# Performance work log

Hardware: AMD Instinct MI355X
Metric: run time of the kernel (lower is better)

Reference implementation:

```python
import jax, jax.numpy as jnp
import numpy as np

D = 100  # embedding_dim (hard-coded in the original module)


def _prelu(x, a):
    return jnp.where(x >= 0, x, a * x)


def setup_inputs() -> dict:
    key = jax.random.key(0)
    ks = jax.random.split(key, 12)
    B, S, L, R, V = 32, 50, 20, 16, 50000
    T = L * R  # tokens per sentence = len_max_sentence * n_routes
    return {
        "stories": jax.random.randint(ks[0], (B, S, T), 0, V),
        "queries": jax.random.randint(ks[1], (B, L), 0, V),
        "emb": 0.1 * jax.random.normal(ks[2], (V, D), dtype=jnp.float32),
        "in_mult": jnp.ones((T, D), dtype=jnp.float32),
        "q_mult": jnp.ones((L, D), dtype=jnp.float32),
        "keys": 0.1 * jax.random.normal(ks[3], (R, D), dtype=jnp.float32),
        "init_state": 0.1 * jax.random.normal(ks[4], (D,), dtype=jnp.float32),
        "U": 0.1 * jax.random.normal(ks[5], (R * D, D), dtype=jnp.float32),
        "Vw": 0.1 * jax.random.normal(ks[6], (R * D, R * D), dtype=jnp.float32),
        "Ww": 0.1 * jax.random.normal(ks[7], (R * D, R * D), dtype=jnp.float32),
        "Hw": 0.1 * jax.random.normal(ks[8], (D, D), dtype=jnp.float32),
        "Rw": 0.1 * jax.random.normal(ks[9], (V, D), dtype=jnp.float32),
        "alpha_in": jnp.ones((1,), dtype=jnp.float32),  # PReLU(init=1)
        "alpha_q": jnp.ones((1,), dtype=jnp.float32),
    }


def reference(stories, queries, emb, in_mult, q_mult, keys, init_state,
              U, Vw, Ww, Hw, Rw, alpha_in, alpha_q):
    B, S, T = stories.shape
    R = keys.shape[0]
    emb0 = emb.at[0].set(0.0)  # padding_idx=0 row is zero
    # stories -> [B,S,T,D] -> route-sum -> [B,S,R,D]
    x = emb0[stories] * in_mult
    x = x.reshape(B, S, R, T // R, D).sum(axis=3)
    # V(keys.flatten()) is constant across timesteps
    v_keys = (keys.reshape(-1) @ Vw.T).reshape(R, D)
    state0 = jnp.tile(init_state[None, None, :], (B, 1, 1))  # [B,1,D]

    def step(state, sent):  # state [B,1,D], sent [B,R,D]
        gate = jax.nn.sigmoid(sent * state + sent * keys)
        u = (state.reshape(B, D) @ U.T).reshape(B, R, D)
        w = (sent.reshape(B, R * D) @ Ww.T).reshape(B, R, D)
        cand = _prelu(u + v_keys + w, alpha_in)
        # null-sentence mask: zero out positions where gate == sigmoid(0) = 0.5
        mask = jax.lax.stop_gradient(jnp.where(gate == 0.5, 0.0, 1.0))
        state = state + (cand * gate * mask).sum(axis=1, keepdims=True)
        # torch.norm over singleton dim=1 (= elementwise abs), kept faithful
        state = state / jnp.sqrt(jnp.sum(state * state, axis=1, keepdims=True))
        return state, None

    state, _ = jax.lax.scan(step, state0, jnp.swapaxes(x, 0, 1))

    q = (emb0[queries] * q_mult).sum(axis=1, keepdims=True)  # [B,1,D]
    h = _prelu(q + (state.reshape(B, D) @ Hw.T).reshape(B, 1, D), alpha_q)
    return h.reshape(B, D) @ Rw.T  # [B, vocab]
```

## Files before the change

kernel.cpp:

```cpp
#include <hip/hip_runtime.h>
#include <cstddef>
#include <cstdint>

#define B_  32
#define S_  50
#define L_  20
#define R_  16
#define D_  100
#define V_  50000
#define T_  320
#define RD_ 1600
#define BS_ 1600
#define NG_ 25
#define NP_ 16

typedef float v4f __attribute__((ext_vector_type(4)));
typedef unsigned short u16;
#define NTL(p)   __builtin_nontemporal_load((const v4f*)(p))

__device__ __forceinline__ void bsplit(float a, unsigned& h, unsigned& l) {
  const unsigned bits = __float_as_uint(a);
  const unsigned hb = bits & 0xffff0000u;
  h = hb >> 16;
  l = __float_as_uint(a - __uint_as_float(hb)) >> 16;
}

__device__ __forceinline__ void bsplit4(float4 a, uint2& h, uint2& l) {
  unsigned h0,h1,h2,h3,l0,l1,l2,l3;
  bsplit(a.x, h0, l0); bsplit(a.y, h1, l1);
  bsplit(a.z, h2, l2); bsplit(a.w, h3, l3);
  h.x = h0 | (h1 << 16); h.y = h2 | (h3 << 16);
  l.x = l0 | (l1 << 16); l.y = l2 | (l3 << 16);
}

__global__ __launch_bounds__(512) void setup_kernel(
    const int* __restrict__ stories, const float* __restrict__ emb,
    const float* __restrict__ in_mult, const float* __restrict__ U,
    const float* __restrict__ Vw, const float* __restrict__ keys,
    const float* __restrict__ init_state, const float* __restrict__ Ww,
    float* __restrict__ x,
    u16* __restrict__ wh, u16* __restrict__ wl,
    float* __restrict__ table, float* __restrict__ vk, float* __restrict__ u0)
{
  const int blk = blockIdx.x, tid = threadIdx.x;
  if (blk < 1600) {
    __shared__ int toks[T_];
    const int* st = stories + (size_t)blk * T_;
    if (tid < T_) toks[tid] = st[tid];
    __syncthreads();
    if (tid < 400) {
      const int j4 = tid * 4;
      const int r  = j4 / D_;
      const int d4 = j4 - r * D_;
      float4 acc = make_float4(0.f, 0.f, 0.f, 0.f);
      #pragma unroll
      for (int l = 0; l < 20; ++l) {
        const int t = r * 20 + l;
        const int tok = toks[t];
        if (tok != 0) {
          float4 e = *(const float4*)&emb[(size_t)tok * D_ + d4];
          float4 m = *(const float4*)&in_mult[(size_t)t * D_ + d4];
          acc.x += e.x * m.x; acc.y += e.y * m.y;
          acc.z += e.z * m.z; acc.w += e.w * m.w;
        }
      }
      float* xo = x + (size_t)blk * RD_;
      xo[(d4 + 0) * 16 + r] = acc.x;
      xo[(d4 + 1) * 16 + r] = acc.y;
      xo[(d4 + 2) * 16 + r] = acc.z;
      xo[(d4 + 3) * 16 + r] = acc.w;
    }
  } else if (blk < 2000) {
    const int qq = blk - 1600;
    const int g = qq >> 4, p = qq & 15;
    const float s0 = (p & 1) ? -1.f : 1.f;
    const float s1 = (p & 2) ? -1.f : 1.f;
    const float s2 = (p & 4) ? -1.f : 1.f;
    const float s3 = (p & 8) ? -1.f : 1.f;
    if (tid < 400) {
      const int d  = tid >> 2;
      const int r0 = (tid & 3) * 4;
      float t[4];
      #pragma unroll
      for (int ri = 0; ri < 4; ++ri) {
        const int orig = (r0 + ri) * D_ + d;
        const float* ur = &U[(size_t)orig * D_ + 4 * g];
        t[ri] = s0*ur[0] + s1*ur[1] + s2*ur[2] + s3*ur[3];
      }
      *(float4*)&table[((size_t)(g * NP_ + p)) * RD_ + tid * 4] =
          make_float4(t[0], t[1], t[2], t[3]);
    }
  } else if (blk < 2200) {
    const int wave = tid >> 6, lane = tid & 63;
    const int jp = (blk - 2000) * 8 + wave;
    const int orig = (jp & 15) * D_ + (jp >> 4);
    float acc = 0.f;
    for (int k = lane; k < RD_; k += 64)
      acc += keys[k] * Vw[(size_t)orig * RD_ + k];
    #pragma unroll
    for (int off = 32; off > 0; off >>= 1) acc += __shfl_down(acc, off);
    if (lane == 0) vk[jp] = acc;
  } else if (blk < 2400) {
    const int wave = tid >> 6, lane = tid & 63;
    const int jp = (blk - 2200) * 8 + wave;
    const int orig = (jp & 15) * D_ + (jp >> 4);
    const float* Ur = U + (size_t)orig * D_;
    float acc = Ur[lane] * init_state[lane];
    if (lane < 36) acc += Ur[64 + lane] * init_state[64 + lane];
    #pragma unroll
    for (int off = 32; off > 0; off >>= 1) acc += __shfl_down(acc, off);
    if (lane == 0) u0[jp] = acc;
  } else {
    const int g   = (blk - 2400) * 512 + tid;
    const int row = g / 200;
    const int rem = g - row * 200;
    const int d   = rem % 100;
    const int r0  = (rem / 100) * 8;
    const int orig = (row & 15) * D_ + (row >> 4);
    const float* src = Ww + (size_t)orig * RD_;
    unsigned h[8], l[8];
    #pragma unroll
    for (int i = 0; i < 8; ++i)
      bsplit(src[(r0 + i) * D_ + d], h[i], l[i]);
    uint4 hv = make_uint4(h[0]|(h[1]<<16), h[2]|(h[3]<<16),
                          h[4]|(h[5]<<16), h[6]|(h[7]<<16));
    uint4 lv = make_uint4(l[0]|(l[1]<<16), l[2]|(l[3]<<16),
                          l[4]|(l[5]<<16), l[6]|(l[7]<<16));
    *(uint4*)&wh[(size_t)row * RD_ + d * 16 + r0] = hv;
    *(uint4*)&wl[(size_t)row * RD_ + d * 16 + r0] = lv;
  }
}

typedef const __attribute__((address_space(1))) unsigned GAu;
typedef __attribute__((address_space(3))) unsigned LDSu;
#define GLL(SRC, DST) __builtin_amdgcn_global_load_lds((GAu*)(SRC), (LDSu*)(DST), 16, 0, 0)

__device__ __forceinline__ void mfma16(v4f& d, v4f a, v4f b) {
  asm("v_mfma_f32_16x16x32_bf16 %0, %1, %2, %0" : "+v"(d) : "v"(a), "v"(b));
}

__global__ __launch_bounds__(512) void gemm_mfma_kernel(
    const float* __restrict__ A,
    const u16* __restrict__ wh, const u16* __restrict__ wl,
    float* __restrict__ C)
{
  __shared__ __align__(16) char smem[2][4][8192];
  const int tid = threadIdx.x;
  const int lane = tid & 63, wid = tid >> 6;
  const int bm = blockIdx.y * 128, bn = blockIdx.x * 128;

  const int brow = wid * 16 + (lane >> 2);
  const int bkb  = (lane & 3) * 16;
  int rb = bn + brow; if (rb > 1599) rb = 1599;
  const int srcB = rb * 3200 + bkb;
  const int ldsB = wid * 1024;
  const char* gwh = (const char*)wh;
  const char* gwl = (const char*)wl;

  int arow[2], awofs[2];
  const int akseg = tid & 7;
  #pragma unroll
  for (int i = 0; i < 2; ++i) {
    const int r = i * 64 + (tid >> 3);
    int ra = bm + r; if (ra > 1599) ra = 1599;
    arow[i] = ra;
    awofs[i] = r * 64 + akseg * 8;
  }

  const int wm = wid >> 2, wn = wid & 3;
  const int r15 = lane & 15, q = lane >> 4;
  const int aoff = (wm * 64 + r15) * 64 + q * 16;
  const int boff = (wn * 32 + r15) * 64 + q * 16;

  v4f acc[4][2];
  #pragma unroll
  for (int i = 0; i < 4; ++i)
    #pragma unroll
    for (int j = 0; j < 2; ++j) acc[i][j] = (v4f)(0.f);

  auto stageB = [&](int buf, int kt) {
    const int kb = kt * 64;
    GLL(gwh + srcB + kb, &smem[buf][2][ldsB]);
    GLL(gwl + srcB + kb, &smem[buf][3][ldsB]);
  };

  float4 a4[2];
  #pragma unroll
  for (int i = 0; i < 2; ++i)
    a4[i] = *(const float4*)&A[(size_t)arow[i] * RD_ + akseg * 4];
  stageB(0, 0);
  #pragma unroll
  for (int i = 0; i < 2; ++i) {
    uint2 h, l; bsplit4(a4[i], h, l);
    *(uint2*)&smem[0][0][awofs[i]] = h;
    *(uint2*)&smem[0][1][awofs[i]] = l;
  }
  __syncthreads();

  for (int kt = 0; kt < 50; ++kt) {
    const int cur = kt & 1;
    if (kt < 49) {
      stageB(cur ^ 1, kt + 1);
      #pragma unroll
      for (int i = 0; i < 2; ++i)
        a4[i] = *(const float4*)&A[(size_t)arow[i] * RD_ + (kt + 1) * 32 + akseg * 4];
    }
    const char* s0 = &smem[cur][0][0];
    v4f ah[4], al[4], bh[2], bl[2];
    #pragma unroll
    for (int t = 0; t < 4; ++t) {
      ah[t] = *(const v4f*)(s0 +         aoff + t * 1024);
      al[t] = *(const v4f*)(s0 +  8192 + aoff + t * 1024);
    }
    #pragma unroll
    for (int t = 0; t < 2; ++t) {
      bh[t] = *(const v4f*)(s0 + 16384 + boff + t * 1024);
      bl[t] = *(const v4f*)(s0 + 24576 + boff + t * 1024);
    }
    #pragma unroll
    for (int im = 0; im < 4; ++im)
      #pragma unroll
      for (int in = 0; in < 2; ++in) {
        mfma16(acc[im][in], ah[im], bh[in]);
        mfma16(acc[im][in], ah[im], bl[in]);
        mfma16(acc[im][in], al[im], bh[in]);
      }
    if (kt < 49) {
      const int nxt = cur ^ 1;
      #pragma unroll
      for (int i = 0; i < 2; ++i) {
        uint2 h, l; bsplit4(a4[i], h, l);
        *(uint2*)&smem[nxt][0][awofs[i]] = h;
        *(uint2*)&smem[nxt][1][awofs[i]] = l;
      }
    }
    __syncthreads();
  }

  const int mb  = bm + wm * 64 + q * 4;
  const int nbq = bn + wn * 32 + r15;
  #pragma unroll
  for (int im = 0; im < 4; ++im) {
    #pragma unroll
    for (int in = 0; in < 2; ++in) {
      const int n = nbq + in * 16;
      const int m0 = mb + im * 16;
      if (n < 1600) {
        #pragma unroll
        for (int r = 0; r < 4; ++r)
          if (m0 + r < 1600)
            C[(size_t)(m0 + r) * RD_ + n] = acc[im][in][r];
      }
    }
  }
}

__global__ __launch_bounds__(448, 2) void scan_kernel(
    const float* __restrict__ x,
    const float* __restrict__ Wall,
    const float* __restrict__ table,
    const float* __restrict__ u0,
    const float* __restrict__ vkeys,
    const float* __restrict__ keys,
    const float* __restrict__ init_state,
    const float* __restrict__ alpha_in_p,
    const int*   __restrict__ queries,
    const float* __restrict__ emb,
    const float* __restrict__ q_mult,
    const float* __restrict__ Hw,
    const float* __restrict__ alpha_q_p,
    float* __restrict__ h_g)
{
  const int b = blockIdx.x, tid = threadIdx.x;
  __shared__ __align__(16) float s_state[D_];
  __shared__ float s_hw[D_ * 101];
  __shared__ __align__(16) unsigned char s_sign[2][112];
  const float alpha = alpha_in_p[0];
  const bool active = (tid < 400);
  const int q4 = tid * 4;
  const int d  = tid >> 2;
  const int r0 = (tid & 3) * 4;
  float kk0 = 0.f, kk1 = 0.f, kk2 = 0.f, kk3 = 0.f;
  float4 vv = make_float4(0.f, 0.f, 0.f, 0.f);
  float state_reg = 0.f;
  const float* xb = x    + (size_t)b * S_ * RD_;
  const float* wb = Wall + (size_t)b * S_ * RD_;
  float4 bx[5], bw[5];
  #pragma unroll
  for (int i = 0; i < 5; ++i) {
    bx[i] = make_float4(0.f, 0.f, 0.f, 0.f);
    bw[i] = make_float4(0.f, 0.f, 0.f, 0.f);
  }
  if (active) {
    kk0 = keys[(r0 + 0) * D_ + d];
    kk1 = keys[(r0 + 1) * D_ + d];
    kk2 = keys[(r0 + 2) * D_ + d];
    kk3 = keys[(r0 + 3) * D_ + d];
    vv = *(const float4*)&vkeys[q4];
    state_reg = init_state[d];
    #pragma unroll
    for (int i = 0; i < 5; ++i) {
      v4f xv = NTL(&xb[(size_t)i * RD_ + q4]);
      v4f wv = NTL(&wb[(size_t)i * RD_ + q4]);
      bx[i] = make_float4(xv.x, xv.y, xv.z, xv.w);
      bw[i] = make_float4(wv.x, wv.y, wv.z, wv.w);
    }
  }
  __syncthreads();

  for (int sg = 0; sg < S_; sg += 5) {
    #pragma unroll
    for (int i = 0; i < 5; ++i) {
      const int s = sg + i;
      if (active) {
        const float4 sent = bx[i], w = bw[i];
        const bool first = (s == 0);
        v4f tv[NG_];
        if (first) {
          tv[0] = *(const v4f*)&u0[q4];
        } else {
          const uint4* sp = (const uint4*)s_sign[s & 1];
          unsigned wd[25];
          uint4 s0v = sp[0]; wd[0]=s0v.x;  wd[1]=s0v.y;  wd[2]=s0v.z;  wd[3]=s0v.w;
          uint4 s1v = sp[1]; wd[4]=s1v.x;  wd[5]=s1v.y;  wd[6]=s1v.z;  wd[7]=s1v.w;
          uint4 s2v = sp[2]; wd[8]=s2v.x;  wd[9]=s2v.y;  wd[10]=s2v.z; wd[11]=s2v.w;
          uint4 s3v = sp[3]; wd[12]=s3v.x; wd[13]=s3v.y; wd[14]=s3v.z; wd[15]=s3v.w;
          uint4 s4v = sp[4]; wd[16]=s4v.x; wd[17]=s4v.y; wd[18]=s4v.z; wd[19]=s4v.w;
          uint4 s5v = sp[5]; wd[20]=s5v.x; wd[21]=s5v.y; wd[22]=s5v.z; wd[23]=s5v.w;
          uint4 s6v = sp[6]; wd[24]=s6v.x;
          #pragma unroll
          for (int g = 0; g < NG_; ++g) {
            const unsigned idx = (wd[g] * 0x01020408u) >> 24;
            tv[g] = *(const v4f*)&table[((size_t)(g * NP_) + idx) * RD_ + q4];
          }
        }
        __builtin_amdgcn_sched_barrier(0);
        if (s + 5 < S_) {
          v4f xv = NTL(&xb[(size_t)(s + 5) * RD_ + q4]);
          v4f wv = NTL(&wb[(size_t)(s + 5) * RD_ + q4]);
          bx[i] = make_float4(xv.x, xv.y, xv.z, xv.w);
          bw[i] = make_float4(wv.x, wv.y, wv.z, wv.w);
        }
        const float sd = state_reg;
        float zx = sent.x * sd + sent.x * kk0;
        float zy = sent.y * sd + sent.y * kk1;
        float zz = sent.z * sd + sent.z * kk2;
        float zw = sent.w * sd + sent.w * kk3;
        float gx = 1.0f / (1.0f + expf(-zx));
        float gy = 1.0f / (1.0f + expf(-zy));
        float gz = 1.0f / (1.0f + expf(-zz));
        float gw = 1.0f / (1.0f + expf(-zw));
        v4f u = tv[0];
        if (!first) {
          #pragma unroll
          for (int g = 1; g < NG_; ++g) {
            u.x += tv[g].x; u.y += tv[g].y; u.z += tv[g].z; u.w += tv[g].w;
          }
        }
        float cx = u.x + vv.x + w.x; cx = cx >= 0.f ? cx : alpha * cx;
        float cy = u.y + vv.y + w.y; cy = cy >= 0.f ? cy : alpha * cy;
        float cz = u.z + vv.z + w.z; cz = cz >= 0.f ? cz : alpha * cz;
        float cw = u.w + vv.w + w.w; cw = cw >= 0.f ? cw : alpha * cw;
        float p  = ((gx == 0.5f) ? 0.f : cx * gx)
                 + ((gy == 0.5f) ? 0.f : cy * gy)
                 + ((gz == 0.5f) ? 0.f : cz * gz)
                 + ((gw == 0.5f) ? 0.f : cw * gw);
        p += __shfl_xor(p, 1);
        p += __shfl_xor(p, 2);
        float v = state_reg + p;
        state_reg = v / sqrtf(v * v);
        if ((tid & 3) == 0) s_sign[(s + 1) & 1][d] = (v < 0.f) ? 1 : 0;
      }
      __syncthreads();
    }
  }

  if (active && (tid & 3) == 0) s_state[d] = state_reg;
  __syncthreads();

  for (int f = tid; f < D_ * D_; f += 448) {
    const int row = f / D_, col = f - row * D_;
    s_hw[row * 101 + col] = Hw[f];
  }
  __syncthreads();
  if (tid < D_) {
    float q = 0.f;
    #pragma unroll
    for (int l = 0; l < L_; ++l) {
      const int tok = queries[b * L_ + l];
      if (tok != 0) q += emb[(size_t)tok * D_ + tid] * q_mult[l * D_ + tid];
    }
    float a = 0.f;
    #pragma unroll 4
    for (int k = 0; k < D_; ++k) a += s_state[k] * s_hw[tid * 101 + k];
    float h = q + a;
    const float aq = alpha_q_p[0];
    h = h >= 0.f ? h : aq * h;
    h_g[(size_t)b * D_ + tid] = h;
  }
}

__global__ __launch_bounds__(256) void out_kernel(
    const float* __restrict__ h_g, const float* __restrict__ Rw, float* __restrict__ out)
{
  __shared__ __align__(16) float sh[B_ * D_];
  __shared__ __align__(16) float sr[32 * D_];
  int tid = threadIdx.x;
  int v0 = blockIdx.x * 32;
  for (int i = tid; i < B_ * D_; i += 256) sh[i] = h_g[i];
  int nrows = V_ - v0; if (nrows > 32) nrows = 32;
  for (int i = tid; i < nrows * D_; i += 256) sr[i] = Rw[(size_t)v0 * D_ + i];
  __syncthreads();
  const float4* sh4 = (const float4*)sh;
  const float4* sr4 = (const float4*)sr;
  int tv = (tid & 15) * 2;
  int tb = (tid >> 4) * 2;
  float a00 = 0.f, a01 = 0.f, a10 = 0.f, a11 = 0.f;
  #pragma unroll
  for (int kc = 0; kc < 25; ++kc) {
    float4 h0 = sh4[tb * 25 + kc];
    float4 h1 = sh4[(tb + 1) * 25 + kc];
    float4 r0 = sr4[tv * 25 + kc];
    float4 r1 = sr4[(tv + 1) * 25 + kc];
    a00 += h0.x*r0.x + h0.y*r0.y + h0.z*r0.z + h0.w*r0.w;
    a01 += h0.x*r1.x + h0.y*r1.y + h0.z*r1.z + h0.w*r1.w;
    a10 += h1.x*r0.x + h1.y*r0.y + h1.z*r0.z + h1.w*r0.w;
    a11 += h1.x*r1.x + h1.y*r1.y + h1.z*r1.z + h1.w*r1.w;
  }
  if (tv < nrows) {
    out[(size_t)tb * V_ + v0 + tv] = a00;
    out[(size_t)(tb + 1) * V_ + v0 + tv] = a10;
  }
  if (tv + 1 < nrows) {
    out[(size_t)tb * V_ + v0 + tv + 1] = a01;
    out[(size_t)(tb + 1) * V_ + v0 + tv + 1] = a11;
  }
}

extern "C" void kernel_launch(void* const* d_in, const int* in_sizes, int n_in,
                              void* d_out, int out_size, void* d_ws, size_t ws_size,
                              hipStream_t stream) {
  const int*   stories    = (const int*)  d_in[0];
  const int*   queries    = (const int*)  d_in[1];
  const float* emb        = (const float*)d_in[2];
  const float* in_mult    = (const float*)d_in[3];
  const float* q_mult     = (const float*)d_in[4];
  const float* keys       = (const float*)d_in[5];
  const float* init_state = (const float*)d_in[6];
  const float* U          = (const float*)d_in[7];
  const float* Vw         = (const float*)d_in[8];
  const float* Ww         = (const float*)d_in[9];
  const float* Hw         = (const float*)d_in[10];
  const float* Rw         = (const float*)d_in[11];
  const float* alpha_in   = (const float*)d_in[12];
  const float* alpha_q    = (const float*)d_in[13];
  float* out = (float*)d_out;

  char* ws = (char*)d_ws;
  float* x     = (float*)(ws);
  float* Wall  = (float*)(ws + 10240000);
  float* table = (float*)(ws + 20480000);
  u16*   wwh   = (u16*)  (ws + 23040000);
  u16*   wwl   = (u16*)  (ws + 28160000);
  float* vk    = (float*)(ws + 33280000);
  float* u0    = (float*)(ws + 33286400);
  float* hbuf  = (float*)(ws + 33292800);

  setup_kernel<<<3025, 512, 0, stream>>>(stories, emb, in_mult, U, Vw, keys,
                                         init_state, Ww, x, wwh, wwl,
                                         table, vk, u0);
  gemm_mfma_kernel<<<dim3(13, 13), 512, 0, stream>>>(x, wwh, wwl, Wall);
  scan_kernel<<<B_, 448, 0, stream>>>(x, Wall, table, u0, vk, keys, init_state,
                                      alpha_in, queries, emb, q_mult, Hw, alpha_q,
                                      hbuf);
  out_kernel<<<(V_ + 31) / 32, 256, 0, stream>>>(hbuf, Rw, out);
}
```

Baseline: 364.9 us.

## Split per-step table gathers across two thread halves in scan kernel

Doubles the scan block to 896 threads and splits the 25 sign-indexed table lookups per step between two groups. The lower 400 threads gather 13 groups, the upper 400 gather the other 12, and the upper group passes its partial sum through shared memory. This halves the serial gather latency per thread on the critical recurrence. In exchange it adds a second barrier per timestep and needs more registers and threads per block.

After: 439.8 us. +20.5%, slower.

```diff
diff --git a/kernel.cpp b/kernel.cpp
--- a/kernel.cpp
+++ b/kernel.cpp
@@ -255,7 +255,7 @@
   }
 }
 
-__global__ __launch_bounds__(448, 2) void scan_kernel(
+__global__ __launch_bounds__(896, 4) void scan_kernel(
     const float* __restrict__ x,
     const float* __restrict__ Wall,
     const float* __restrict__ table,
@@ -274,36 +274,34 @@
   const int b = blockIdx.x, tid = threadIdx.x;
   __shared__ __align__(16) float s_state[D_];
   __shared__ float s_hw[D_ * 101];
+  __shared__ __align__(16) float s_u[RD_];
   __shared__ __align__(16) unsigned char s_sign[2][112];
   const float alpha = alpha_in_p[0];
-  const bool active = (tid < 400);
-  const int q4 = tid * 4;
+  const bool lower = (tid < 400);
+  const bool upper = (tid >= 448 && tid < 848);
+  const int lj4 = tid * 4;
+  const int uj4 = (tid - 448) * 4;
   const int d  = tid >> 2;
   const int r0 = (tid & 3) * 4;
   float kk0 = 0.f, kk1 = 0.f, kk2 = 0.f, kk3 = 0.f;
-  float4 vv = make_float4(0.f, 0.f, 0.f, 0.f);
+  v4f vv = (v4f)(0.f);
   float state_reg = 0.f;
   const float* xb = x    + (size_t)b * S_ * RD_;
   const float* wb = Wall + (size_t)b * S_ * RD_;
-  float4 bx[5], bw[5];
-  #pragma unroll
-  for (int i = 0; i < 5; ++i) {
-    bx[i] = make_float4(0.f, 0.f, 0.f, 0.f);
-    bw[i] = make_float4(0.f, 0.f, 0.f, 0.f);
-  }
-  if (active) {
+  v4f bx[5], bw[5];
+  #pragma unroll
+  for (int i = 0; i < 5; ++i) { bx[i] = (v4f)(0.f); bw[i] = (v4f)(0.f); }
+  if (lower) {
     kk0 = keys[(r0 + 0) * D_ + d];
     kk1 = keys[(r0 + 1) * D_ + d];
     kk2 = keys[(r0 + 2) * D_ + d];
     kk3 = keys[(r0 + 3) * D_ + d];
-    vv = *(const float4*)&vkeys[q4];
+    vv = *(const v4f*)&vkeys[lj4];
     state_reg = init_state[d];
     #pragma unroll
     for (int i = 0; i < 5; ++i) {
-      v4f xv = NTL(&xb[(size_t)i * RD_ + q4]);
-      v4f wv = NTL(&wb[(size_t)i * RD_ + q4]);
-      bx[i] = make_float4(xv.x, xv.y, xv.z, xv.w);
-      bw[i] = make_float4(wv.x, wv.y, wv.z, wv.w);
+      bx[i] = NTL(&xb[(size_t)i * RD_ + lj4]);
+      bw[i] = NTL(&wb[(size_t)i * RD_ + lj4]);
     }
   }
   __syncthreads();
@@ -312,59 +310,87 @@
     #pragma unroll
     for (int i = 0; i < 5; ++i) {
       const int s = sg + i;
-      if (active) {
-        const float4 sent = bx[i], w = bw[i];
-        const bool first = (s == 0);
-        v4f tv[NG_];
+      const bool first = (s == 0);
+      v4f u_own = (v4f)(0.f);
+      v4f sent = (v4f)(0.f), w = (v4f)(0.f);
+      float gx = 0.f, gy = 0.f, gz = 0.f, gw_ = 0.f;
+      if (lower) {
+        sent = bx[i]; w = bw[i];
+        v4f tv[13];
         if (first) {
-          tv[0] = *(const v4f*)&u0[q4];
+          tv[0] = *(const v4f*)&u0[lj4];
         } else {
           const uint4* sp = (const uint4*)s_sign[s & 1];
-          unsigned wd[25];
+          unsigned wd[13];
           uint4 s0v = sp[0]; wd[0]=s0v.x;  wd[1]=s0v.y;  wd[2]=s0v.z;  wd[3]=s0v.w;
           uint4 s1v = sp[1]; wd[4]=s1v.x;  wd[5]=s1v.y;  wd[6]=s1v.z;  wd[7]=s1v.w;
           uint4 s2v = sp[2]; wd[8]=s2v.x;  wd[9]=s2v.y;  wd[10]=s2v.z; wd[11]=s2v.w;
-          uint4 s3v = sp[3]; wd[12]=s3v.x; wd[13]=s3v.y; wd[14]=s3v.z; wd[15]=s3v.w;
-          uint4 s4v = sp[4]; wd[16]=s4v.x; wd[17]=s4v.y; wd[18]=s4v.z; wd[19]=s4v.w;
-          uint4 s5v = sp[5]; wd[20]=s5v.x; wd[21]=s5v.y; wd[22]=s5v.z; wd[23]=s5v.w;
-          uint4 s6v = sp[6]; wd[24]=s6v.x;
+          wd[12] = sp[3].x;
           #pragma unroll
-          for (int g = 0; g < NG_; ++g) {
+          for (int g = 0; g < 13; ++g) {
             const unsigned idx = (wd[g] * 0x01020408u) >> 24;
-            tv[g] = *(const v4f*)&table[((size_t)(g * NP_) + idx) * RD_ + q4];
+            tv[g] = *(const v4f*)&table[((size_t)(g * NP_) + idx) * RD_ + lj4];
           }
         }
         __builtin_amdgcn_sched_barrier(0);
         if (s + 5 < S_) {
-          v4f xv = NTL(&xb[(size_t)(s + 5) * RD_ + q4]);
-          v4f wv = NTL(&wb[(size_t)(s + 5) * RD_ + q4]);
-          bx[i] = make_float4(xv.x, xv.y, xv.z, xv.w);
-          bw[i] = make_float4(wv.x, wv.y, wv.z, wv.w);
+          bx[i] = NTL(&xb[(size_t)(s + 5) * RD_ + lj4]);
+          bw[i] = NTL(&wb[(size_t)(s + 5) * RD_ + lj4]);
         }
         const float sd = state_reg;
         float zx = sent.x * sd + sent.x * kk0;
         float zy = sent.y * sd + sent.y * kk1;
         float zz = sent.z * sd + sent.z * kk2;
         float zw = sent.w * sd + sent.w * kk3;
-        float gx = 1.0f / (1.0f + expf(-zx));
-        float gy = 1.0f / (1.0f + expf(-zy));
-        float gz = 1.0f / (1.0f + expf(-zz));
-        float gw = 1.0f / (1.0f + expf(-zw));
-        v4f u = tv[0];
+        gx  = 1.0f / (1.0f + expf(-zx));
+        gy  = 1.0f / (1.0f + expf(-zy));
+        gz  = 1.0f / (1.0f + expf(-zz));
+        gw_ = 1.0f / (1.0f + expf(-zw));
+        u_own = tv[0];
         if (!first) {
           #pragma unroll
-          for (int g = 1; g < NG_; ++g) {
-            u.x += tv[g].x; u.y += tv[g].y; u.z += tv[g].z; u.w += tv[g].w;
+          for (int g = 1; g < 13; ++g) {
+            u_own.x += tv[g].x; u_own.y += tv[g].y;
+            u_own.z += tv[g].z; u_own.w += tv[g].w;
           }
+        }
+      }
+      if (upper && !first) {
+        const uint4* sp = (const uint4*)s_sign[s & 1];
+        uint4 s3v = sp[3], s4v = sp[4], s5v = sp[5], s6v = sp[6];
+        unsigned wd[12];
+        wd[0]=s3v.y;  wd[1]=s3v.z;  wd[2]=s3v.w;
+        wd[3]=s4v.x;  wd[4]=s4v.y;  wd[5]=s4v.z;  wd[6]=s4v.w;
+        wd[7]=s5v.x;  wd[8]=s5v.y;  wd[9]=s5v.z;  wd[10]=s5v.w;
+        wd[11]=s6v.x;
+        v4f tu[12];
+        #pragma unroll
+        for (int k = 0; k < 12; ++k) {
+          const unsigned idx = (wd[k] * 0x01020408u) >> 24;
+          tu[k] = *(const v4f*)&table[((size_t)((13 + k) * NP_) + idx) * RD_ + uj4];
+        }
+        v4f su = tu[0];
+        #pragma unroll
+        for (int k = 1; k < 12; ++k) {
+          su.x += tu[k].x; su.y += tu[k].y; su.z += tu[k].z; su.w += tu[k].w;
+        }
+        *(v4f*)&s_u[uj4] = su;
+      }
+      __syncthreads();
+      if (lower) {
+        v4f u = u_own;
+        if (!first) {
+          v4f uu = *(const v4f*)&s_u[lj4];
+          u.x += uu.x; u.y += uu.y; u.z += uu.z; u.w += uu.w;
         }
         float cx = u.x + vv.x + w.x; cx = cx >= 0.f ? cx : alpha * cx;
         float cy = u.y + vv.y + w.y; cy = cy >= 0.f ? cy : alpha * cy;
         float cz = u.z + vv.z + w.z; cz = cz >= 0.f ? cz : alpha * cz;
         float cw = u.w + vv.w + w.w; cw = cw >= 0.f ? cw : alpha * cw;
-        float p  = ((gx == 0.5f) ? 0.f : cx * gx)
-                 + ((gy == 0.5f) ? 0.f : cy * gy)
-                 + ((gz == 0.5f) ? 0.f : cz * gz)
-                 + ((gw == 0.5f) ? 0.f : cw * gw);
+        float p  = ((gx  == 0.5f) ? 0.f : cx * gx)
+                 + ((gy  == 0.5f) ? 0.f : cy * gy)
+                 + ((gz  == 0.5f) ? 0.f : cz * gz)
+                 + ((gw_ == 0.5f) ? 0.f : cw * gw_);
         p += __shfl_xor(p, 1);
         p += __shfl_xor(p, 2);
         float v = state_reg + p;
@@ -375,10 +401,10 @@
     }
   }
 
-  if (active && (tid & 3) == 0) s_state[d] = state_reg;
+  if (lower && (tid & 3) == 0) s_state[d] = state_reg;
   __syncthreads();
 
-  for (int f = tid; f < D_ * D_; f += 448) {
+  for (int f = tid; f < D_ * D_; f += 896) {
     const int row = f / D_, col = f - row * D_;
     s_hw[row * 101 + col] = Hw[f];
   }
@@ -470,7 +496,7 @@
                                          init_state, Ww, x, wwh, wwl,
                                          table, vk, u0);
   gemm_mfma_kernel<<<dim3(13, 13), 512, 0, stream>>>(x, wwh, wwl, Wall);
-  scan_kernel<<<B_, 448, 0, stream>>>(x, Wall, table, u0, vk, keys, init_state,
+  scan_kernel<<<B_, 896, 0, stream>>>(x, Wall, table, u0, vk, keys, init_state,
                                       alpha_in, queries, emb, q_mult, Hw, alpha_q,
                                       hbuf);
   out_kernel<<<(V_ + 31) / 32, 256, 0, stream>>>(hbuf, Rw, out);
```
